# Kernel tuning notes

Hardware: AMD Instinct MI355X
Metric: run time of the kernel (lower is better)

The kernel has to match this reference:

```python
import jax, jax.numpy as jnp
import numpy as np

B, C, N = 16, 256, 1024
D_QK, D_V, BINS = 64, 256, 32
EPS = 1e-5


def setup_inputs() -> dict:
    key = jax.random.key(0)
    ks = jax.random.split(key, 12)

    def xavier(k, shape):
        fan_in, fan_out = shape[1], shape[0]
        lim = (6.0 / (fan_in + fan_out)) ** 0.5
        return jax.random.uniform(k, shape, jnp.float32, -lim, lim)

    return {
        "x": jax.random.normal(ks[0], (B, C, N), jnp.float32),
        "discrete": jax.random.randint(ks[1], (B, N, 3), 0, BINS),
        "xyz": jax.random.uniform(ks[2], (B, N, 3), jnp.float32),
        "q_w": xavier(ks[3], (D_QK, C)),
        "k_w": xavier(ks[4], (D_QK, C)),
        "v_w": xavier(ks[5], (D_V, C)),
        "v_b": jnp.zeros((D_V,), jnp.float32),
        "trans_w": xavier(ks[6], (C, D_V)),
        "trans_b": jnp.zeros((C,), jnp.float32),
        "bn_gamma": jnp.ones((C,), jnp.float32),
        "bn_beta": jnp.zeros((C,), jnp.float32),
        "x_lt": xavier(ks[7], (2 * BINS - 1, D_QK)),
        "y_lt": xavier(ks[8], (2 * BINS - 1, D_QK)),
        "z_lt": xavier(ks[9], (2 * BINS - 1, D_QK)),
    }


def reference(x, discrete, xyz, q_w, k_w, v_w, v_b, trans_w, trans_b,
              bn_gamma, bn_beta, x_lt, y_lt, z_lt):
    # x: [B,C,N], discrete: [B,N,3] int bin coords in [0,BINS)
    n = x.shape[2]
    x_q = jnp.einsum('dc,bcn->bnd', q_w, x)                      # [B,N,d_qk]
    x_k = jnp.einsum('dc,bcn->bdn', k_w, x)                      # [B,d_qk,N]
    x_v = jnp.einsum('dc,bcn->bdn', v_w, x) + v_b[None, :, None]  # [B,d_v,N]

    energy = jnp.einsum('bnd,bdm->bnm', x_q, x_k)                # [B,N,N]

    def rel_term(lt, d):
        # q @ lookup-table then gather along relative bin index (irregular access)
        ql = jnp.einsum('bnd,rd->bnr', x_q, lt)                  # [B,N,2*BINS-1]
        idx = d[:, None, :] - d[:, :, None] + (BINS - 1)          # [B,N,N]
        return jnp.take_along_axis(ql, idx, axis=2)

    dx, dy, dz = discrete[..., 0], discrete[..., 1], discrete[..., 2]
    energy = energy + rel_term(x_lt, dx) + rel_term(y_lt, dy) + rel_term(z_lt, dz)

    energy = energy / (float(n) ** 0.5)                           # scale == 'root'
    attention = jax.nn.softmax(energy, axis=-1)

    x_r = jnp.einsum('bdn,bnm->bdm', x_v, attention)              # [B,d_v,N]

    # offset=True: trans_conv(x - x_r) -> BN (batch stats) -> ReLU -> residual
    h = x - x_r
    t = jnp.einsum('cd,bdn->bcn', trans_w, h) + trans_b[None, :, None]
    mean = t.mean(axis=(0, 2), keepdims=True)
    var = t.var(axis=(0, 2), keepdims=True)
    t = (t - mean) * jax.lax.rsqrt(var + EPS)
    t = t * bn_gamma[None, :, None] + bn_beta[None, :, None]
    x_r = jax.nn.relu(t)
    return x + x_r
```

## Files before the change

### kernel.cpp

```cpp
#include <hip/hip_runtime.h>
#include <math.h>

#define BB 16
#define CC 256
#define NN 1024
#define DQK_ 64
#define DV_ 256
#define NR 192
#define EPS_F 1e-5f

#define OFF_XT  ((size_t)0)
#define OFF_QB  ((size_t)2097152)
#define OFF_KB  ((size_t)2621440)
#define OFF_QL  ((size_t)3145728)
#define OFF_HT  ((size_t)2097152)
#define OFF_VB  ((size_t)6291456)
#define OFF_ATT ((size_t)8388608)
#define OFF_T   ((size_t)8388608)
#define OFF_WQK ((size_t)16777216)
#define OFF_WV  ((size_t)16793600)
#define OFF_WT  ((size_t)16826368)
#define OFF_LTB ((size_t)16859136)
#define OFF_BNS ((size_t)16865280)
#define OFF_BNQ ((size_t)16865536)

typedef __attribute__((ext_vector_type(8))) short short8;
typedef __attribute__((ext_vector_type(4))) float f32x4;

__device__ __forceinline__ unsigned short f2b(float f) {
    unsigned int u = __float_as_uint(f);
    u = u + 0x7fffu + ((u >> 16) & 1u);
    return (unsigned short)(u >> 16);
}
__device__ __forceinline__ float b2f(unsigned short s) {
    return __uint_as_float(((unsigned int)s) << 16);
}

__global__ __launch_bounds__(256) void k_prep(
    const float* __restrict__ qw, const float* __restrict__ kw,
    const float* __restrict__ vw, const float* __restrict__ tw,
    const float* __restrict__ xlt, const float* __restrict__ ylt,
    const float* __restrict__ zlt,
    unsigned short* __restrict__ Wqk, unsigned short* __restrict__ Wv,
    unsigned short* __restrict__ Wt, unsigned short* __restrict__ LTb,
    float* __restrict__ bnS, float* __restrict__ bnQ)
{
    if (blockIdx.x == 160) {
        bnS[threadIdx.x] = 0.f;
        bnQ[threadIdx.x] = 0.f;
        return;
    }
    if (blockIdx.x > 160) {
        const int o2 = (blockIdx.x - 161) * 256 + threadIdx.x;
        const int e = o2 * 4;
        const int r = e >> 6, d = e & 63;
        const int a = r >> 6, q = r & 63;
        ushort4 u;
        if (q < 63) {
            const float* lt = (a == 0) ? xlt : ((a == 1) ? ylt : zlt);
            const float4 v = *(const float4*)(lt + q * 64 + d);
            u.x = f2b(v.x); u.y = f2b(v.y); u.z = f2b(v.z); u.w = f2b(v.w);
        } else {
            u.x = u.y = u.z = u.w = 0;
        }
        *(ushort4*)(LTb + e) = u;
        return;
    }
    const int o = blockIdx.x * 256 + threadIdx.x;
    const float* src; unsigned short* dst;
    if (o < 8192) {
        const int e = o * 4;
        src = (e < 16384) ? (qw + e) : (kw + e - 16384);
        dst = Wqk + e;
    } else if (o < 24576) {
        const int e = (o - 8192) * 4;
        src = vw + e; dst = Wv + e;
    } else {
        const int e = (o - 24576) * 4;
        src = tw + e; dst = Wt + e;
    }
    const float4 v = *(const float4*)src;
    ushort4 u;
    u.x = f2b(v.x); u.y = f2b(v.y); u.z = f2b(v.z); u.w = f2b(v.w);
    *(ushort4*)dst = u;
}

__global__ __launch_bounds__(256) void k_xt(
    const float* __restrict__ x, unsigned short* __restrict__ xT)
{
    __shared__ float tile[64][68];
    const int b = blockIdx.z;
    const int c0 = blockIdx.y * 64;
    const int n0 = blockIdx.x * 64;
    const int tid = threadIdx.x;
    #pragma unroll
    for (int it = 0; it < 4; ++it) {
        const int r = it * 16 + (tid >> 4);
        const int c4 = (tid & 15) * 4;
        *(float4*)&tile[r][c4] =
            *(const float4*)(x + ((size_t)b * CC + c0 + r) * NN + n0 + c4);
    }
    __syncthreads();
    const int n = tid >> 2;
    const int cg = (tid & 3) * 16;
    alignas(16) unsigned short buf[16];
    #pragma unroll
    for (int j = 0; j < 16; ++j) buf[j] = f2b(tile[cg + j][n]);
    unsigned short* dst = xT + ((size_t)b * NN + n0 + n) * CC + c0 + cg;
    *(short8*)dst       = *(const short8*)&buf[0];
    *(short8*)(dst + 8) = *(const short8*)&buf[8];
}

__global__ __launch_bounds__(256) void k_projqk(
    const unsigned short* __restrict__ xT, const unsigned short* __restrict__ Wqk,
    unsigned short* __restrict__ Qb, unsigned short* __restrict__ Kb)
{
    const int b = blockIdx.y;
    const int n0 = blockIdx.x * 32;
    const int tid = threadIdx.x;
    const int l = tid & 63, w = tid >> 6;
    const int l15 = l & 15, l4 = l >> 4;
    const int ng = (w >> 1) * 16, wh = (w & 1) * 64;
    const unsigned short* ap = xT + ((size_t)b * NN + n0 + ng + l15) * CC + l4 * 8;
    const unsigned short* bp = Wqk + ((size_t)(wh + l15)) * CC + l4 * 8;
    f32x4 z = {0.f, 0.f, 0.f, 0.f};
    f32x4 acc[4] = {z, z, z, z};
    #pragma unroll 2
    for (int kk = 0; kk < CC; kk += 32) {
        const short8 a = *(const short8*)(ap + kk);
        short8 bf[4];
        #pragma unroll
        for (int j = 0; j < 4; ++j)
            bf[j] = *(const short8*)(bp + (size_t)j * 16 * CC + kk);
        #pragma unroll
        for (int j = 0; j < 4; ++j)
            acc[j] = __builtin_amdgcn_mfma_f32_16x16x32_bf16(a, bf[j], acc[j], 0, 0, 0);
    }
    #pragma unroll
    for (int j = 0; j < 4; ++j)
        #pragma unroll
        for (int r = 0; r < 4; ++r) {
            const int n = n0 + ng + l4 * 4 + r;
            const int ch = wh + j * 16 + l15;
            const unsigned short v = f2b(acc[j][r]);
            if (ch < 64) Qb[((size_t)b * NN + n) * DQK_ + ch] = v;
            else         Kb[((size_t)b * NN + n) * DQK_ + ch - 64] = v;
        }
}

__global__ __launch_bounds__(256) void k_qlm(
    const unsigned short* __restrict__ Qb, const unsigned short* __restrict__ LTb,
    float* __restrict__ QL)
{
    const int b = blockIdx.y;
    const int n0 = blockIdx.x * 64;
    const int tid = threadIdx.x;
    const int l = tid & 63, w = tid >> 6;
    const int l15 = l & 15, l4 = l >> 4;
    const unsigned short* ap = Qb + ((size_t)b * NN + n0 + w * 16 + l15) * DQK_ + l4 * 8;
    const short8 a0 = *(const short8*)ap;
    const short8 a1 = *(const short8*)(ap + 32);
    f32x4 z = {0.f, 0.f, 0.f, 0.f};
    f32x4 acc[12];
    #pragma unroll
    for (int j = 0; j < 12; ++j) acc[j] = z;
    #pragma unroll
    for (int j = 0; j < 12; ++j) {
        const unsigned short* bp = LTb + (size_t)(j * 16 + l15) * DQK_ + l4 * 8;
        const short8 b0 = *(const short8*)bp;
        const short8 b1 = *(const short8*)(bp + 32);
        acc[j] = __builtin_amdgcn_mfma_f32_16x16x32_bf16(a0, b0, acc[j], 0, 0, 0);
        acc[j] = __builtin_amdgcn_mfma_f32_16x16x32_bf16(a1, b1, acc[j], 0, 0, 0);
    }
    float* qrow0 = QL + ((size_t)b * NN + n0 + w * 16 + l4 * 4) * NR;
    #pragma unroll
    for (int rr = 0; rr < 4; ++rr) {
        float* qr = qrow0 + (size_t)rr * NR + l15;
        #pragma unroll
        for (int j = 0; j < 12; ++j) qr[j * 16] = acc[j][rr];
    }
}

__global__ __launch_bounds__(256) void k_projv(
    const unsigned short* __restrict__ Wv, const unsigned short* __restrict__ xT,
    const float* __restrict__ vb, unsigned short* __restrict__ Vb)
{
    const int b = blockIdx.y;
    const int n0 = blockIdx.x * 32;
    const int tid = threadIdx.x;
    const int l = tid & 63, w = tid >> 6;
    const int l15 = l & 15, l4 = l >> 4;
    const unsigned short* ap = Wv + ((size_t)(w * 64 + l15)) * CC + l4 * 8;
    const unsigned short* bp = xT + ((size_t)b * NN + n0 + l15) * CC + l4 * 8;
    f32x4 z = {0.f, 0.f, 0.f, 0.f};
    f32x4 acc[4][2] = {{z, z}, {z, z}, {z, z}, {z, z}};
    #pragma unroll 2
    for (int kk = 0; kk < CC; kk += 32) {
        short8 af[4], bf[2];
        #pragma unroll
        for (int i = 0; i < 4; ++i)
            af[i] = *(const short8*)(ap + (size_t)i * 16 * CC + kk);
        #pragma unroll
        for (int j = 0; j < 2; ++j)
            bf[j] = *(const short8*)(bp + (size_t)j * 16 * CC + kk);
        #pragma unroll
        for (int i = 0; i < 4; ++i)
            #pragma unroll
            for (int j = 0; j < 2; ++j)
                acc[i][j] = __builtin_amdgcn_mfma_f32_16x16x32_bf16(af[i], bf[j], acc[i][j], 0, 0, 0);
    }
    #pragma unroll
    for (int i = 0; i < 4; ++i)
        #pragma unroll
        for (int r = 0; r < 4; ++r) {
            const int dv = w * 64 + i * 16 + l4 * 4 + r;
            const float bias = vb[dv];
            #pragma unroll
            for (int j = 0; j < 2; ++j) {
                const int n = n0 + j * 16 + l15;
                Vb[((size_t)b * DV_ + dv) * NN + n] = f2b(acc[i][j][r] + bias);
            }
        }
}

__global__ __launch_bounds__(512) void k_attn(
    const unsigned short* __restrict__ Qb, const unsigned short* __restrict__ Kb,
    const float* __restrict__ QL, const int* __restrict__ disc,
    unsigned short* __restrict__ att)
{
    __shared__ float QLs[16][193];
    __shared__ int   dmp[1024];
    __shared__ float redM[8][16];
    __shared__ float redS[8][16];
    const int b = blockIdx.y;
    const int q0 = blockIdx.x * 16;
    const int tid = threadIdx.x;
    const int l = tid & 63, w = tid >> 6;
    const int l15 = l & 15, l4 = l >> 4;

    for (int o = tid; o < 16 * NR; o += 512) {
        const int r = o / NR, c = o - r * NR;
        QLs[r][c] = QL[((size_t)b * NN + q0 + r) * NR + c];
    }
    for (int m = tid; m < NN; m += 512) {
        const size_t base = ((size_t)b * NN + m) * 3;
        dmp[m] = disc[base] | (disc[base + 1] << 8) | (disc[base + 2] << 16);
    }
    __syncthreads();

    const int q = q0 + l15;
    const int dn0 = disc[((size_t)b * NN + q) * 3 + 0] - 31;
    const int dn1 = disc[((size_t)b * NN + q) * 3 + 1] - 31;
    const int dn2 = disc[((size_t)b * NN + q) * 3 + 2] - 31;

    const unsigned short* qp = Qb + ((size_t)b * NN + q) * DQK_ + l4 * 8;
    const short8 qf0 = *(const short8*)qp;
    const short8 qf1 = *(const short8*)(qp + 32);

    const unsigned short* kbase = Kb + (size_t)b * NN * DQK_ + l4 * 8;
    const unsigned short* kp0 = kbase + (size_t)(w * 16 + l15) * DQK_;
    short8 kf0 = *(const short8*)kp0;
    short8 kf1 = *(const short8*)(kp0 + 32);

    float s[32];
    #pragma unroll
    for (int t = 0; t < 8; ++t) {
        const int tn = (t < 7) ? t + 1 : 7;
        const unsigned short* kpn = kbase + (size_t)(tn * 128 + w * 16 + l15) * DQK_;
        const short8 nf0 = *(const short8*)kpn;
        const short8 nf1 = *(const short8*)(kpn + 32);
        f32x4 acc = {0.f, 0.f, 0.f, 0.f};
        acc = __builtin_amdgcn_mfma_f32_16x16x32_bf16(kf0, qf0, acc, 0, 0, 0);
        acc = __builtin_amdgcn_mfma_f32_16x16x32_bf16(kf1, qf1, acc, 0, 0, 0);
        const int m0 = t * 128 + w * 16 + l4 * 4;
        #pragma unroll
        for (int r = 0; r < 4; ++r) {
            const int pm = dmp[m0 + r];
            const int i0 = (pm & 255) - dn0;
            const int i1 = ((pm >> 8) & 255) - dn1;
            const int i2 = (pm >> 16) - dn2;
            const float rel = QLs[l15][i0] + QLs[l15][64 + i1] + QLs[l15][128 + i2];
            s[t * 4 + r] = (acc[r] + rel) * 0.03125f;
        }
        kf0 = nf0; kf1 = nf1;
    }

    float mx = -1e30f;
    #pragma unroll
    for (int i = 0; i < 32; ++i) mx = fmaxf(mx, s[i]);
    mx = fmaxf(mx, __shfl_xor(mx, 16));
    mx = fmaxf(mx, __shfl_xor(mx, 32));
    if (l < 16) redM[w][l] = mx;
    __syncthreads();
    mx = redM[0][l15];
    #pragma unroll
    for (int ww = 1; ww < 8; ++ww) mx = fmaxf(mx, redM[ww][l15]);

    float sum = 0.f;
    #pragma unroll
    for (int i = 0; i < 32; ++i) { s[i] = __expf(s[i] - mx); sum += s[i]; }
    sum += __shfl_xor(sum, 16);
    sum += __shfl_xor(sum, 32);
    if (l < 16) redS[w][l] = sum;
    __syncthreads();
    float tot = redS[0][l15];
    #pragma unroll
    for (int ww = 1; ww < 8; ++ww) tot += redS[ww][l15];
    const float inv = 1.0f / tot;

    #pragma unroll
    for (int t = 0; t < 8; ++t)
        #pragma unroll
        for (int r = 0; r < 4; ++r) {
            const int m = t * 128 + w * 16 + l4 * 4 + r;
            att[((size_t)b * NN + m) * NN + q] = f2b(s[t * 4 + r] * inv);
        }
}

__global__ __launch_bounds__(256) void k_pv(
    const unsigned short* __restrict__ att, const unsigned short* __restrict__ Vb,
    const unsigned short* __restrict__ xT, unsigned short* __restrict__ HT)
{
    __shared__ unsigned short As[2][128][72];
    __shared__ unsigned short Bs[2][128][72];
    const int b = blockIdx.z;
    const int d0 = blockIdx.y * 128;
    const int m0 = blockIdx.x * 128;
    const int tid = threadIdx.x;
    const int l = tid & 63, w = tid >> 6;
    const int l15 = l & 15, l4 = l >> 4;
    const int wm = (w & 1) * 64, wd = (w >> 1) * 64;

    const unsigned short* agbase = att + ((size_t)b * NN + m0) * NN;
    const unsigned short* bgbase = Vb + ((size_t)b * DV_ + d0) * NN;

    f32x4 z = {0.f, 0.f, 0.f, 0.f};
    f32x4 acc[4][4];
    #pragma unroll
    for (int i = 0; i < 4; ++i)
        #pragma unroll
        for (int j = 0; j < 4; ++j) acc[i][j] = z;

    short8 pa[4], pb[4];
    #pragma unroll
    for (int it = 0; it < 4; ++it) {
        const int f = it * 256 + tid, r = f >> 3, c = (f & 7) * 8;
        pa[it] = *(const short8*)(agbase + (size_t)r * NN + c);
        pb[it] = *(const short8*)(bgbase + (size_t)r * NN + c);
    }
    #pragma unroll
    for (int it = 0; it < 4; ++it) {
        const int f = it * 256 + tid, r = f >> 3, c = (f & 7) * 8;
        *(short8*)&As[0][r][c] = pa[it];
        *(short8*)&Bs[0][r][c] = pb[it];
    }
    __syncthreads();

    for (int ks = 0; ks < 16; ++ks) {
        const int cur = ks & 1;
        if (ks < 15) {
            const int nk = (ks + 1) * 64;
            #pragma unroll
            for (int it = 0; it < 4; ++it) {
                const int f = it * 256 + tid, r = f >> 3, c = (f & 7) * 8;
                pa[it] = *(const short8*)(agbase + (size_t)r * NN + nk + c);
                pb[it] = *(const short8*)(bgbase + (size_t)r * NN + nk + c);
            }
        }
        #pragma unroll
        for (int ksub = 0; ksub < 2; ++ksub) {
            short8 af[4], bf[4];
            #pragma unroll
            for (int i = 0; i < 4; ++i)
                af[i] = *(const short8*)&As[cur][wm + i * 16 + l15][ksub * 32 + l4 * 8];
            #pragma unroll
            for (int j = 0; j < 4; ++j)
                bf[j] = *(const short8*)&Bs[cur][wd + j * 16 + l15][ksub * 32 + l4 * 8];
            #pragma unroll
            for (int i = 0; i < 4; ++i)
                #pragma unroll
                for (int j = 0; j < 4; ++j)
                    acc[i][j] = __builtin_amdgcn_mfma_f32_16x16x32_bf16(af[i], bf[j], acc[i][j], 0, 0, 0);
        }
        if (ks < 15) {
            #pragma unroll
            for (int it = 0; it < 4; ++it) {
                const int f = it * 256 + tid, r = f >> 3, c = (f & 7) * 8;
                *(short8*)&As[cur ^ 1][r][c] = pa[it];
                *(short8*)&Bs[cur ^ 1][r][c] = pb[it];
            }
        }
        __syncthreads();
    }

    #pragma unroll
    for (int i = 0; i < 4; ++i)
        #pragma unroll
        for (int r = 0; r < 4; ++r) {
            const int m = m0 + wm + i * 16 + l4 * 4 + r;
            const unsigned short* xrow = xT + ((size_t)b * NN + m) * CC;
            unsigned short* hrow = HT + ((size_t)b * NN + m) * CC;
            #pragma unroll
            for (int j = 0; j < 4; ++j) {
                const int dv = d0 + wd + j * 16 + l15;
                hrow[dv] = f2b(b2f(xrow[dv]) - acc[i][j][r]);
            }
        }
}

__global__ __launch_bounds__(256) void k_trans(
    const unsigned short* __restrict__ Wt, const unsigned short* __restrict__ HT,
    const float* __restrict__ tb, unsigned short* __restrict__ T,
    float* __restrict__ bnS, float* __restrict__ bnQ)
{
    __shared__ float sS[128], sQ[128];
    const int b = blockIdx.z;
    const int c0 = blockIdx.y * 128;
    const int n0 = blockIdx.x * 64;
    const int tid = threadIdx.x;
    const int l = tid & 63, w = tid >> 6;
    const int l15 = l & 15, l4 = l >> 4;
    const int wc = (w & 1) * 64, wn = (w >> 1) * 32;
    if (tid < 128) { sS[tid] = 0.f; sQ[tid] = 0.f; }
    __syncthreads();
    const unsigned short* ap = Wt + ((size_t)(c0 + wc + l15)) * CC + l4 * 8;
    const unsigned short* bp = HT + ((size_t)b * NN + n0 + wn + l15) * CC + l4 * 8;
    f32x4 z = {0.f, 0.f, 0.f, 0.f};
    f32x4 acc[4][2] = {{z, z}, {z, z}, {z, z}, {z, z}};
    #pragma unroll 2
    for (int kk = 0; kk < CC; kk += 32) {
        short8 af[4], bf[2];
        #pragma unroll
        for (int i = 0; i < 4; ++i)
            af[i] = *(const short8*)(ap + (size_t)i * 16 * CC + kk);
        #pragma unroll
        for (int j = 0; j < 2; ++j)
            bf[j] = *(const short8*)(bp + (size_t)j * 16 * CC + kk);
        #pragma unroll
        for (int i = 0; i < 4; ++i)
            #pragma unroll
            for (int j = 0; j < 2; ++j)
                acc[i][j] = __builtin_amdgcn_mfma_f32_16x16x32_bf16(af[i], bf[j], acc[i][j], 0, 0, 0);
    }
    #pragma unroll
    for (int i = 0; i < 4; ++i)
        #pragma unroll
        for (int r = 0; r < 4; ++r) {
            const int cl = wc + i * 16 + l4 * 4 + r;
            const int c = c0 + cl;
            const float bias = tb[c];
            float s = 0.f, q = 0.f;
            #pragma unroll
            for (int j = 0; j < 2; ++j) {
                const int n = n0 + wn + j * 16 + l15;
                const float t = acc[i][j][r] + bias;
                T[((size_t)b * CC + c) * NN + n] = f2b(t);
                s += t; q += t * t;
            }
            s += __shfl_xor(s, 1); s += __shfl_xor(s, 2);
            s += __shfl_xor(s, 4); s += __shfl_xor(s, 8);
            q += __shfl_xor(q, 1); q += __shfl_xor(q, 2);
            q += __shfl_xor(q, 4); q += __shfl_xor(q, 8);
            if (l15 == 0) {
                atomicAdd(&sS[cl], s);
                atomicAdd(&sQ[cl], q);
            }
        }
    __syncthreads();
    if (tid < 128) {
        atomicAdd(&bnS[c0 + tid], sS[tid]);
        atomicAdd(&bnQ[c0 + tid], sQ[tid]);
    }
}

__global__ __launch_bounds__(256) void k_out(
    const float* __restrict__ x, const unsigned short* __restrict__ T,
    const float* __restrict__ gamma, const float* __restrict__ beta,
    const float* __restrict__ bnS, const float* __restrict__ bnQ,
    float* __restrict__ out)
{
    const int i8 = blockIdx.x * 256 + threadIdx.x;
    const int c = (i8 >> 7) & 255;
    const float meanv = bnS[c] * (1.0f / 16384.0f);
    const float varv  = bnQ[c] * (1.0f / 16384.0f) - meanv * meanv;
    const float inv   = rsqrtf(varv + EPS_F);
    const float g = gamma[c] * inv;
    const float be = beta[c];
    const short8 t8 = *(const short8*)(T + (size_t)i8 * 8);
    const unsigned short* tp = (const unsigned short*)&t8;
    const float4 xa = *(const float4*)(x + (size_t)i8 * 8);
    const float4 xb = *(const float4*)(x + (size_t)i8 * 8 + 4);
    float4 oa, ob;
    oa.x = xa.x + fmaxf(g * (b2f(tp[0]) - meanv) + be, 0.0f);
    oa.y = xa.y + fmaxf(g * (b2f(tp[1]) - meanv) + be, 0.0f);
    oa.z = xa.z + fmaxf(g * (b2f(tp[2]) - meanv) + be, 0.0f);
    oa.w = xa.w + fmaxf(g * (b2f(tp[3]) - meanv) + be, 0.0f);
    ob.x = xb.x + fmaxf(g * (b2f(tp[4]) - meanv) + be, 0.0f);
    ob.y = xb.y + fmaxf(g * (b2f(tp[5]) - meanv) + be, 0.0f);
    ob.z = xb.z + fmaxf(g * (b2f(tp[6]) - meanv) + be, 0.0f);
    ob.w = xb.w + fmaxf(g * (b2f(tp[7]) - meanv) + be, 0.0f);
    *(float4*)(out + (size_t)i8 * 8)     = oa;
    *(float4*)(out + (size_t)i8 * 8 + 4) = ob;
}

extern "C" void kernel_launch(void* const* d_in, const int* in_sizes, int n_in,
                              void* d_out, int out_size, void* d_ws, size_t ws_size,
                              hipStream_t stream)
{
    const float* x     = (const float*)d_in[0];
    const int*   disc  = (const int*)d_in[1];
    const float* qw    = (const float*)d_in[3];
    const float* kw    = (const float*)d_in[4];
    const float* vw    = (const float*)d_in[5];
    const float* vb    = (const float*)d_in[6];
    const float* tw    = (const float*)d_in[7];
    const float* tb    = (const float*)d_in[8];
    const float* gamma = (const float*)d_in[9];
    const float* beta  = (const float*)d_in[10];
    const float* xlt   = (const float*)d_in[11];
    const float* ylt   = (const float*)d_in[12];
    const float* zlt   = (const float*)d_in[13];
    float* ws  = (float*)d_ws;
    float* out = (float*)d_out;

    unsigned short* xT  = (unsigned short*)(ws + OFF_XT);
    unsigned short* Qb  = (unsigned short*)(ws + OFF_QB);
    unsigned short* Kbf = (unsigned short*)(ws + OFF_KB);
    float*          QL  = ws + OFF_QL;
    unsigned short* HT  = (unsigned short*)(ws + OFF_HT);
    unsigned short* Vb  = (unsigned short*)(ws + OFF_VB);
    unsigned short* ATT = (unsigned short*)(ws + OFF_ATT);
    unsigned short* T   = (unsigned short*)(ws + OFF_T);
    unsigned short* Wqk = (unsigned short*)(ws + OFF_WQK);
    unsigned short* Wv  = (unsigned short*)(ws + OFF_WV);
    unsigned short* Wt  = (unsigned short*)(ws + OFF_WT);
    unsigned short* LTb = (unsigned short*)(ws + OFF_LTB);
    float*          bnS = ws + OFF_BNS;
    float*          bnQ = ws + OFF_BNQ;

    k_prep  <<<dim3(173), 256, 0, stream>>>(qw, kw, vw, tw, xlt, ylt, zlt,
                                            Wqk, Wv, Wt, LTb, bnS, bnQ);
    k_xt    <<<dim3(16, 4, 16), 256, 0, stream>>>(x, xT);
    k_projqk<<<dim3(32, 16), 256, 0, stream>>>(xT, Wqk, Qb, Kbf);
    k_qlm   <<<dim3(16, 16), 256, 0, stream>>>(Qb, LTb, QL);
    k_projv <<<dim3(32, 16), 256, 0, stream>>>(Wv, xT, vb, Vb);
    k_attn  <<<dim3(64, 16), 512, 0, stream>>>(Qb, Kbf, QL, disc, ATT);
    k_pv    <<<dim3(8, 2, 16), 256, 0, stream>>>(ATT, Vb, xT, HT);
    k_trans <<<dim3(16, 2, 16), 256, 0, stream>>>(Wt, HT, tb, T, bnS, bnQ);
    k_out   <<<dim3(2048), 256, 0, stream>>>(x, T, gamma, beta, bnS, bnQ, out);
}
```

Baseline: 133.6 us.

## Fuse trans conv, BN stats and output into one cooperative kernel with grid barrier

Replaces the separate trans-conv and BN/output kernels with a single cooperative kernel. Each block keeps its GEMM accumulators in registers, adds its BN partial sums atomically, waits at a global atomic barrier, then normalizes and writes the output directly. This avoids writing and re-reading the T intermediate and saves one launch. In exchange it adds a grid-wide spin barrier and depends on cooperative launch, falling back to the old two kernels if that launch fails.

```diff
diff --git a/kernel.cpp b/kernel.cpp
--- a/kernel.cpp
+++ b/kernel.cpp
@@ -16,13 +16,14 @@
 #define OFF_HT  ((size_t)2097152)
 #define OFF_VB  ((size_t)6291456)
 #define OFF_ATT ((size_t)8388608)
-#define OFF_T   ((size_t)8388608)
 #define OFF_WQK ((size_t)16777216)
 #define OFF_WV  ((size_t)16793600)
 #define OFF_WT  ((size_t)16826368)
 #define OFF_LTB ((size_t)16859136)
 #define OFF_BNS ((size_t)16865280)
 #define OFF_BNQ ((size_t)16865536)
+#define OFF_BAR ((size_t)16865792)
+#define OFF_T   ((size_t)16866048)
 
 typedef __attribute__((ext_vector_type(8))) short short8;
 typedef __attribute__((ext_vector_type(4))) float f32x4;
@@ -43,11 +44,13 @@
     const float* __restrict__ zlt,
     unsigned short* __restrict__ Wqk, unsigned short* __restrict__ Wv,
     unsigned short* __restrict__ Wt, unsigned short* __restrict__ LTb,
-    float* __restrict__ bnS, float* __restrict__ bnQ)
+    float* __restrict__ bnS, float* __restrict__ bnQ,
+    unsigned int* __restrict__ bar)
 {
     if (blockIdx.x == 160) {
         bnS[threadIdx.x] = 0.f;
         bnQ[threadIdx.x] = 0.f;
+        if (threadIdx.x == 0) *bar = 0u;
         return;
     }
     if (blockIdx.x > 160) {
@@ -102,11 +105,11 @@
     }
     __syncthreads();
     const int n = tid >> 2;
-    const int cg = (tid & 3) * 16;
+    const int cg2 = (tid & 3) * 16;
     alignas(16) unsigned short buf[16];
     #pragma unroll
-    for (int j = 0; j < 16; ++j) buf[j] = f2b(tile[cg + j][n]);
-    unsigned short* dst = xT + ((size_t)b * NN + n0 + n) * CC + c0 + cg;
+    for (int j = 0; j < 16; ++j) buf[j] = f2b(tile[cg2 + j][n]);
+    unsigned short* dst = xT + ((size_t)b * NN + n0 + n) * CC + c0 + cg2;
     *(short8*)dst       = *(const short8*)&buf[0];
     *(short8*)(dst + 8) = *(const short8*)&buf[8];
 }
@@ -404,6 +407,113 @@
             for (int j = 0; j < 4; ++j) {
                 const int dv = d0 + wd + j * 16 + l15;
                 hrow[dv] = f2b(b2f(xrow[dv]) - acc[i][j][r]);
+            }
+        }
+}
+
+__global__ __launch_bounds__(256) void k_tout(
+    const unsigned short* __restrict__ Wt, const unsigned short* __restrict__ HT,
+    const float* __restrict__ tb, const float* __restrict__ x,
+    const float* __restrict__ gamma, const float* __restrict__ beta,
+    float* __restrict__ bnS, float* __restrict__ bnQ,
+    unsigned int* __restrict__ bar, float* __restrict__ out)
+{
+    __shared__ float sS[128], sQ[128], sM[128];
+    const int bx = blockIdx.x & 15;
+    const int by = (blockIdx.x >> 4) & 1;
+    const int b  = blockIdx.x >> 5;
+    const int c0 = by * 128;
+    const int n0 = bx * 64;
+    const int tid = threadIdx.x;
+    const int l = tid & 63, w = tid >> 6;
+    const int l15 = l & 15, l4 = l >> 4;
+    const int wc = (w & 1) * 64, wn = (w >> 1) * 32;
+    if (tid < 128) { sS[tid] = 0.f; sQ[tid] = 0.f; }
+    __syncthreads();
+    const unsigned short* ap = Wt + ((size_t)(c0 + wc + l15)) * CC + l4 * 8;
+    const unsigned short* bp = HT + ((size_t)b * NN + n0 + wn + l15) * CC + l4 * 8;
+    f32x4 z = {0.f, 0.f, 0.f, 0.f};
+    f32x4 acc[4][2] = {{z, z}, {z, z}, {z, z}, {z, z}};
+    #pragma unroll 2
+    for (int kk = 0; kk < CC; kk += 32) {
+        short8 af[4], bf[2];
+        #pragma unroll
+        for (int i = 0; i < 4; ++i)
+            af[i] = *(const short8*)(ap + (size_t)i * 16 * CC + kk);
+        #pragma unroll
+        for (int j = 0; j < 2; ++j)
+            bf[j] = *(const short8*)(bp + (size_t)j * 16 * CC + kk);
+        #pragma unroll
+        for (int i = 0; i < 4; ++i)
+            #pragma unroll
+            for (int j = 0; j < 2; ++j)
+                acc[i][j] = __builtin_amdgcn_mfma_f32_16x16x32_bf16(af[i], bf[j], acc[i][j], 0, 0, 0);
+    }
+    #pragma unroll
+    for (int i = 0; i < 4; ++i)
+        #pragma unroll
+        for (int r = 0; r < 4; ++r) {
+            const int cl = wc + i * 16 + l4 * 4 + r;
+            const float bias = tb[c0 + cl];
+            float s = 0.f, q = 0.f;
+            #pragma unroll
+            for (int j = 0; j < 2; ++j) {
+                const float t = acc[i][j][r] + bias;
+                s += t; q += t * t;
+            }
+            s += __shfl_xor(s, 1); s += __shfl_xor(s, 2);
+            s += __shfl_xor(s, 4); s += __shfl_xor(s, 8);
+            q += __shfl_xor(q, 1); q += __shfl_xor(q, 2);
+            q += __shfl_xor(q, 4); q += __shfl_xor(q, 8);
+            if (l15 == 0) {
+                atomicAdd(&sS[cl], s);
+                atomicAdd(&sQ[cl], q);
+            }
+        }
+    __syncthreads();
+    if (tid < 128) {
+        atomicAdd(&bnS[c0 + tid], sS[tid]);
+        atomicAdd(&bnQ[c0 + tid], sQ[tid]);
+    }
+    __syncthreads();
+
+    if (tid == 0) {
+        __threadfence();
+        __hip_atomic_fetch_add(bar, 1u, __ATOMIC_ACQ_REL, __HIP_MEMORY_SCOPE_AGENT);
+        while (__hip_atomic_load(bar, __ATOMIC_ACQUIRE, __HIP_MEMORY_SCOPE_AGENT)
+               < (unsigned int)gridDim.x) {
+            __builtin_amdgcn_s_sleep(8);
+        }
+    }
+    __syncthreads();
+
+    if (tid < 128) {
+        const float S  = __hip_atomic_load(&bnS[c0 + tid], __ATOMIC_RELAXED,
+                                           __HIP_MEMORY_SCOPE_AGENT);
+        const float Qv = __hip_atomic_load(&bnQ[c0 + tid], __ATOMIC_RELAXED,
+                                           __HIP_MEMORY_SCOPE_AGENT);
+        const float mean = S * (1.0f / 16384.0f);
+        const float var  = Qv * (1.0f / 16384.0f) - mean * mean;
+        sS[tid] = gamma[c0 + tid] * rsqrtf(var + EPS_F);
+        sQ[tid] = beta[c0 + tid];
+        sM[tid] = mean;
+    }
+    __syncthreads();
+
+    #pragma unroll
+    for (int i = 0; i < 4; ++i)
+        #pragma unroll
+        for (int r = 0; r < 4; ++r) {
+            const int cl = wc + i * 16 + l4 * 4 + r;
+            const int c = c0 + cl;
+            const float bias = tb[c];
+            const float g = sS[cl], be = sQ[cl], mean = sM[cl];
+            #pragma unroll
+            for (int j = 0; j < 2; ++j) {
+                const int n = n0 + wn + j * 16 + l15;
+                const float t = acc[i][j][r] + bias;
+                const size_t off = ((size_t)b * CC + c) * NN + n;
+                out[off] = x[off] + fmaxf(g * (t - mean) + be, 0.0f);
             }
         }
 }
@@ -537,15 +647,24 @@
     unsigned short* LTb = (unsigned short*)(ws + OFF_LTB);
     float*          bnS = ws + OFF_BNS;
     float*          bnQ = ws + OFF_BNQ;
+    unsigned int*   bar = (unsigned int*)(ws + OFF_BAR);
 
     k_prep  <<<dim3(173), 256, 0, stream>>>(qw, kw, vw, tw, xlt, ylt, zlt,
-                                            Wqk, Wv, Wt, LTb, bnS, bnQ);
+                                            Wqk, Wv, Wt, LTb, bnS, bnQ, bar);
     k_xt    <<<dim3(16, 4, 16), 256, 0, stream>>>(x, xT);
     k_projqk<<<dim3(32, 16), 256, 0, stream>>>(xT, Wqk, Qb, Kbf);
     k_qlm   <<<dim3(16, 16), 256, 0, stream>>>(Qb, LTb, QL);
     k_projv <<<dim3(32, 16), 256, 0, stream>>>(Wv, xT, vb, Vb);
     k_attn  <<<dim3(64, 16), 512, 0, stream>>>(Qb, Kbf, QL, disc, ATT);
     k_pv    <<<dim3(8, 2, 16), 256, 0, stream>>>(ATT, Vb, xT, HT);
-    k_trans <<<dim3(16, 2, 16), 256, 0, stream>>>(Wt, HT, tb, T, bnS, bnQ);
-    k_out   <<<dim3(2048), 256, 0, stream>>>(x, T, gamma, beta, bnS, bnQ, out);
-}
+
+    void* args[] = { (void*)&Wt, (void*)&HT, (void*)&tb, (void*)&x,
+                     (void*)&gamma, (void*)&beta, (void*)&bnS,
+                     (void*)&bnQ, (void*)&bar, (void*)&out };
+    hipError_t cerr = hipLaunchCooperativeKernel(
+        (void*)k_tout, dim3(512), dim3(256), args, 0, stream);
+    if (cerr != hipSuccess) {
+        k_trans<<<dim3(16, 2, 16), 256, 0, stream>>>(Wt, HT, tb, T, bnS, bnQ);
+        k_out  <<<dim3(2048), 256, 0, stream>>>(x, T, gamma, beta, bnS, bnQ, out);
+    }
+}
```

New measurement: 180.9 us. 1.35x slower.
